# Performance work log

Hardware: AMD Instinct MI355X
Metric: run time of the kernel (lower is better)

## Reference

```python
import jax, jax.numpy as jnp
import numpy as np

NEG_SLOPE = 0.01  # torch F.leaky_relu default used in the DGL GAT-style layer


def grat_layer(h, src, dst, W, a, n_nodes):
    """One GRAT (GAT-style) layer.
    h: [N, d_in], src/dst: [E] int, W: [d_in, d_out], a: [2*d_out] (attn_fc weight
    on concat [z_src || z_dst]). Returns [N, d_out].
    """
    d_out = W.shape[1]
    z = h @ W                                   # [N, d_out]
    # attention logits per edge: a^T [z_src || z_dst]
    s_src = z @ a[:d_out]                       # [N]
    s_dst = z @ a[d_out:]                       # [N]
    e = jax.nn.leaky_relu(s_src[src] + s_dst[dst], NEG_SLOPE)  # [E]
    # numerically stable softmax over incoming edges of each dst node
    m = jax.ops.segment_max(e, dst, num_segments=n_nodes)      # [N]
    m = jnp.where(jnp.isfinite(m), m, 0.0)      # nodes with no in-edges
    w = jnp.exp(e - m[dst])                     # [E]
    denom = jax.ops.segment_sum(w, dst, num_segments=n_nodes)  # [N]
    alpha = w / jnp.maximum(denom, 1e-9)[dst]   # [E]
    # weighted scatter-aggregate of source features into dst
    out = jax.ops.segment_sum(alpha[:, None] * z[src], dst, num_segments=n_nodes)
    return out                                  # [N, d_out]


def setup_inputs() -> dict:
    key = jax.random.key(0)
    ks = jax.random.split(key, 10)
    N, E = 100000, 1600000
    IN, H1, H2, OUT = 128, 32, 32, 1
    feature = jax.random.normal(ks[0], (N, IN), dtype=jnp.float32)
    src = jax.random.randint(ks[1], (E,), 0, N, dtype=jnp.int32)
    dst = jax.random.randint(ks[2], (E,), 0, N, dtype=jnp.int32)
    s = 0.1
    W1 = jax.random.normal(ks[3], (IN, H1), dtype=jnp.float32) * s
    a1 = jax.random.normal(ks[4], (2 * H1,), dtype=jnp.float32) * s
    W2 = jax.random.normal(ks[5], (H1, H2), dtype=jnp.float32) * s
    a2 = jax.random.normal(ks[6], (2 * H2,), dtype=jnp.float32) * s
    W3 = jax.random.normal(ks[7], (H2, OUT), dtype=jnp.float32) * s
    a3 = jax.random.normal(ks[8], (2 * OUT,), dtype=jnp.float32) * s
    return {"feature": feature, "src": src, "dst": dst,
            "W1": W1, "a1": a1, "W2": W2, "a2": a2, "W3": W3, "a3": a3}


def reference(feature, src, dst, W1, a1, W2, a2, W3, a3):
    n = feature.shape[0]
    h = jax.nn.relu(grat_layer(feature, src, dst, W1, a1, n))
    h = jax.nn.relu(grat_layer(h, src, dst, W2, a2, n))
    h = grat_layer(h, src, dst, W3, a3, n)
    return jax.nn.sigmoid(h)                    # [N, 1]
```

## Files before the change

### kernel.cpp

```cpp
#include <hip/hip_runtime.h>
#include <hip/hip_bf16.h>
#include <cstdint>
#include <cstddef>

#define NEG_SLOPE 0.01f

static __device__ __forceinline__ unsigned short f2bf(float f) {
    __hip_bfloat16 b = __float2bfloat16(f);
    return *(unsigned short*)&b;
}
static __device__ __forceinline__ float bf2f(unsigned short u) {
    __hip_bfloat16 b = *(__hip_bfloat16*)&u;
    return __bfloat162float(b);
}


__global__ __launch_bounds__(128) void gemm1_kernel(
    const float* __restrict__ h, const float* __restrict__ W,
    const float* __restrict__ a, unsigned short* __restrict__ zb,
    float* __restrict__ s_src, float* __restrict__ s_dst, int N)
{
    __shared__ float Wl[128 * 32];
    int tid = threadIdx.x;
    int rowBase = blockIdx.x * 64;

    {
        const float4* W4 = (const float4*)W;
        float4* Wl4 = (float4*)Wl;
        for (int i = tid; i < 1024; i += 128) Wl4[i] = W4[i];
    }
    __syncthreads();

    int wv   = tid >> 6;
    int lane = tid & 63;
    int g    = lane >> 3;
    int l8   = lane & 7;
    int r0   = wv * 32 + g * 4;
    int col4 = l8 * 4;

    float acc[4][4];
#pragma unroll
    for (int i = 0; i < 4; i++)
#pragma unroll
        for (int c = 0; c < 4; c++) acc[i][c] = 0.f;

    const float4* h4  = (const float4*)h;
    const float4* Wl4 = (const float4*)Wl;

    size_t rowOff[4];
#pragma unroll
    for (int i = 0; i < 4; i++) {
        int r = rowBase + r0 + i;
        rowOff[i] = (size_t)((r < N) ? r : (N - 1)) * 32;
    }

#pragma unroll 2
    for (int kq = 0; kq < 32; kq++) {
        float4 w0 = Wl4[(kq * 4 + 0) * 8 + l8];
        float4 w1 = Wl4[(kq * 4 + 1) * 8 + l8];
        float4 w2 = Wl4[(kq * 4 + 2) * 8 + l8];
        float4 w3 = Wl4[(kq * 4 + 3) * 8 + l8];
#pragma unroll
        for (int i = 0; i < 4; i++) {
            float4 hv = h4[rowOff[i] + kq];
            acc[i][0] += hv.x * w0.x; acc[i][1] += hv.x * w0.y;
            acc[i][2] += hv.x * w0.z; acc[i][3] += hv.x * w0.w;
            acc[i][0] += hv.y * w1.x; acc[i][1] += hv.y * w1.y;
            acc[i][2] += hv.y * w1.z; acc[i][3] += hv.y * w1.w;
            acc[i][0] += hv.z * w2.x; acc[i][1] += hv.z * w2.y;
            acc[i][2] += hv.z * w2.z; acc[i][3] += hv.z * w2.w;
            acc[i][0] += hv.w * w3.x; acc[i][1] += hv.w * w3.y;
            acc[i][2] += hv.w * w3.z; acc[i][3] += hv.w * w3.w;
        }
    }

    float4 alo = ((const float4*)a)[l8];
    float4 ahi = ((const float4*)a)[8 + l8];
#pragma unroll
    for (int i = 0; i < 4; i++) {
        int row = rowBase + r0 + i;
        if (row < N) {
            ushort4 zv4 = make_ushort4(f2bf(acc[i][0]), f2bf(acc[i][1]),
                                       f2bf(acc[i][2]), f2bf(acc[i][3]));
            *(ushort4*)&zb[(size_t)row * 32 + col4] = zv4;
            float ps = acc[i][0] * alo.x + acc[i][1] * alo.y + acc[i][2] * alo.z + acc[i][3] * alo.w;
            float pd = acc[i][0] * ahi.x + acc[i][1] * ahi.y + acc[i][2] * ahi.z + acc[i][3] * ahi.w;
            ps += __shfl_xor(ps, 1, 64); ps += __shfl_xor(ps, 2, 64); ps += __shfl_xor(ps, 4, 64);
            pd += __shfl_xor(pd, 1, 64); pd += __shfl_xor(pd, 2, 64); pd += __shfl_xor(pd, 4, 64);
            if (l8 == 0) { s_src[row] = ps; s_dst[row] = pd; }
        }
    }
}

__global__ __launch_bounds__(128) void gemm2_kernel(
    const float* __restrict__ h, const float* __restrict__ W,
    const float* __restrict__ a, unsigned short* __restrict__ zb,
    float* __restrict__ s_src, float* __restrict__ s_dst, int N)
{
    __shared__ float Hl[64 * 44];
    __shared__ float Wl[32 * 32];
    int tid = threadIdx.x;
    int rowBase = blockIdx.x * 64;

    {
        const float4* W4 = (const float4*)W;
        float4* Wl4 = (float4*)Wl;
        for (int i = tid; i < 256; i += 128) Wl4[i] = W4[i];
    }
    {
        const float4* h4 = (const float4*)h;
        for (int i = tid; i < 64 * 8; i += 128) {
            int r = i >> 3, kq = i & 7;
            float4 v = (rowBase + r < N) ? h4[(size_t)(rowBase + r) * 8 + kq]
                                         : make_float4(0.f, 0.f, 0.f, 0.f);
            *(float4*)&Hl[r * 44 + kq * 4] = v;
        }
    }
    __syncthreads();

    int wv   = tid >> 6;
    int lane = tid & 63;
    int g    = lane >> 3;
    int l8   = lane & 7;
    int r0   = wv * 32 + g * 4;
    int col4 = l8 * 4;

    float acc[4][4];
#pragma unroll
    for (int i = 0; i < 4; i++)
#pragma unroll
        for (int c = 0; c < 4; c++) acc[i][c] = 0.f;

    const float4* H4  = (const float4*)Hl;
    const float4* Wl4 = (const float4*)Wl;

#pragma unroll
    for (int kq = 0; kq < 8; kq++) {
        float4 w0 = Wl4[(kq * 4 + 0) * 8 + l8];
        float4 w1 = Wl4[(kq * 4 + 1) * 8 + l8];
        float4 w2 = Wl4[(kq * 4 + 2) * 8 + l8];
        float4 w3 = Wl4[(kq * 4 + 3) * 8 + l8];
#pragma unroll
        for (int i = 0; i < 4; i++) {
            float4 hv = H4[(r0 + i) * 11 + kq];
            acc[i][0] += hv.x * w0.x; acc[i][1] += hv.x * w0.y;
            acc[i][2] += hv.x * w0.z; acc[i][3] += hv.x * w0.w;
            acc[i][0] += hv.y * w1.x; acc[i][1] += hv.y * w1.y;
            acc[i][2] += hv.y * w1.z; acc[i][3] += hv.y * w1.w;
            acc[i][0] += hv.z * w2.x; acc[i][1] += hv.z * w2.y;
            acc[i][2] += hv.z * w2.z; acc[i][3] += hv.z * w2.w;
            acc[i][0] += hv.w * w3.x; acc[i][1] += hv.w * w3.y;
            acc[i][2] += hv.w * w3.z; acc[i][3] += hv.w * w3.w;
        }
    }

    float4 alo = ((const float4*)a)[l8];
    float4 ahi = ((const float4*)a)[8 + l8];
#pragma unroll
    for (int i = 0; i < 4; i++) {
        int row = rowBase + r0 + i;
        if (row < N) {
            ushort4 zv4 = make_ushort4(f2bf(acc[i][0]), f2bf(acc[i][1]),
                                       f2bf(acc[i][2]), f2bf(acc[i][3]));
            *(ushort4*)&zb[(size_t)row * 32 + col4] = zv4;
            float ps = acc[i][0] * alo.x + acc[i][1] * alo.y + acc[i][2] * alo.z + acc[i][3] * alo.w;
            float pd = acc[i][0] * ahi.x + acc[i][1] * ahi.y + acc[i][2] * ahi.z + acc[i][3] * ahi.w;
            ps += __shfl_xor(ps, 1, 64); ps += __shfl_xor(ps, 2, 64); ps += __shfl_xor(ps, 4, 64);
            pd += __shfl_xor(pd, 1, 64); pd += __shfl_xor(pd, 2, 64); pd += __shfl_xor(pd, 4, 64);
            if (l8 == 0) { s_src[row] = ps; s_dst[row] = pd; }
        }
    }
}

__global__ __launch_bounds__(256) void gemm3_kernel(
    const float* __restrict__ h, const float* __restrict__ W,
    const float* __restrict__ a, float2* __restrict__ zs,
    float* __restrict__ s_dst, int N)
{
    int i = blockIdx.x * 256 + threadIdx.x;
    if (i >= N) return;
    const float4* hp = (const float4*)(h + (size_t)i * 32);
    const float4* wp = (const float4*)W;
    float acc = 0.f;
#pragma unroll
    for (int c = 0; c < 8; c++) {
        float4 v = hp[c];
        float4 w = wp[c];
        acc += v.x * w.x + v.y * w.y + v.z * w.z + v.w * w.w;
    }
    zs[i] = make_float2(acc, acc * a[0]);
    s_dst[i] = acc * a[1];
}


#define TILE_E 4096
#define NB_MAX 512

__global__ __launch_bounds__(256) void csr_hist_kernel(
    const int* __restrict__ dst, int* __restrict__ counts,
    int E, int TB, int NB)
{
    __shared__ int hist[NB_MAX];
    int tid = threadIdx.x;
    int t = blockIdx.x;
    for (int b = tid; b < NB; b += 256) hist[b] = 0;
    __syncthreads();
    int base = t * TILE_E;
    for (int i = tid; i < TILE_E; i += 256) {
        int k = base + i;
        if (k < E) atomicAdd(&hist[dst[k] >> 8], 1);
    }
    __syncthreads();
    for (int b = tid; b < NB; b += 256) counts[b * TB + t] = hist[b];
}

__global__ __launch_bounds__(256) void scan1_kernel(
    const int* __restrict__ vals, int* __restrict__ incl,
    int* __restrict__ blockSums, int M)
{
    __shared__ int tmp[256];
    int tid = threadIdx.x;
    int i = blockIdx.x * 256 + tid;
    int v = (i < M) ? vals[i] : 0;
    tmp[tid] = v;
    __syncthreads();
#pragma unroll
    for (int off = 1; off < 256; off <<= 1) {
        int t = (tid >= off) ? tmp[tid - off] : 0;
        __syncthreads();
        tmp[tid] += t;
        __syncthreads();
    }
    if (i < M) incl[i] = tmp[tid];
    if (tid == 255) blockSums[blockIdx.x] = tmp[255];
}

__global__ __launch_bounds__(1024) void scan2_kernel(int* __restrict__ blockSums, int nb)
{
    __shared__ int tmp[1024];
    int tid = threadIdx.x;
    int v = (tid < nb) ? blockSums[tid] : 0;
    tmp[tid] = v;
    __syncthreads();
#pragma unroll
    for (int off = 1; off < 1024; off <<= 1) {
        int t = (tid >= off) ? tmp[tid - off] : 0;
        __syncthreads();
        tmp[tid] += t;
        __syncthreads();
    }
    if (tid < nb) blockSums[tid] = tmp[tid] - v;
}

__global__ __launch_bounds__(256) void scan3_kernel(
    const int* __restrict__ vals, const int* __restrict__ blockSums,
    int* __restrict__ cscan, int M, int E)
{
    int i = blockIdx.x * 256 + threadIdx.x;
    if (i < M) {
        cscan[i] = cscan[i] - vals[i] + blockSums[i >> 8];
    }
    if (i == 0) cscan[M] = E;
}

__global__ __launch_bounds__(256) void csr_scatter_kernel(
    const int* __restrict__ src, const int* __restrict__ dst,
    const int* __restrict__ cscan, int* __restrict__ ebuf,
    int E, int TB, int NB)
{
    __shared__ int baseB[NB_MAX];
    __shared__ int cur[NB_MAX];
    int tid = threadIdx.x;
    int t = blockIdx.x;
    for (int b = tid; b < NB; b += 256) {
        baseB[b] = cscan[b * TB + t];
        cur[b] = 0;
    }
    __syncthreads();
    int base = t * TILE_E;
    for (int i = tid; i < TILE_E; i += 256) {
        int k = base + i;
        if (k < E) {
            int d = dst[k], s = src[k];
            int b = d >> 8;
            int r = atomicAdd(&cur[b], 1);
            ebuf[baseB[b] + r] = (s << 8) | (d & 255);
        }
    }
}

__global__ __launch_bounds__(256) void csr_bucket_kernel(
    const int* __restrict__ ebuf, const int* __restrict__ cscan,
    int* __restrict__ csr_src, int* __restrict__ offsets,
    int N, int E, int TB)
{
    __shared__ int eb[8192];
    __shared__ int hist[256];
    __shared__ int loff[256];
    __shared__ int tmp[256];
    int tid = threadIdx.x;
    int b = blockIdx.x;

    int beg = cscan[b * TB];
    int endv = cscan[(b + 1) * TB];
    int cnt = endv - beg;
    int first = b << 8;

    hist[tid] = 0;
    __syncthreads();

    bool inLds = (cnt <= 8192);
    for (int i = tid; i < cnt; i += 256) {
        int v = ebuf[beg + i];
        if (inLds) eb[i] = v;
        atomicAdd(&hist[v & 255], 1);
    }
    __syncthreads();

    int hv = hist[tid];
    tmp[tid] = hv;
    __syncthreads();
#pragma unroll
    for (int off = 1; off < 256; off <<= 1) {
        int t = (tid >= off) ? tmp[tid - off] : 0;
        __syncthreads();
        tmp[tid] += t;
        __syncthreads();
    }
    loff[tid] = tmp[tid] - hv;
    __syncthreads();

    if (first + tid < N) offsets[first + tid] = beg + loff[tid];
    if (b == 0 && tid == 0) offsets[N] = E;

    hist[tid] = 0;
    __syncthreads();

    for (int i = tid; i < cnt; i += 256) {
        int v = inLds ? eb[i] : ebuf[beg + i];
        int d8 = v & 255;
        int r = atomicAdd(&hist[d8], 1);
        csr_src[beg + loff[d8] + r] = v >> 8;
    }
}


__global__ __launch_bounds__(256) void agg32_fused_kernel(
    const int* __restrict__ offsets, const int* __restrict__ csr_src,
    const float* __restrict__ s_src, const float* __restrict__ s_dst,
    const unsigned short* __restrict__ zb, float* __restrict__ h, int N)
{
    __shared__ float2 wsbuf[8 * 128];
    int g    = threadIdx.x >> 5;
    int lane = threadIdx.x & 31;
    int node = blockIdx.x * 8 + g;
    if (node >= N) return;
    float2* ws = &wsbuf[g * 128];

    int beg = offsets[node], end = offsets[node + 1];
    int deg = end - beg;
    float sd = s_dst[node];
    float o = 0.f;
    float rden;

    if (deg <= 128) {
        int   sreg[4];
        float ev[4];
        int nIter = (deg + 31) >> 5;
        float m = -3.0e38f;
#pragma unroll 4
        for (int it = 0; it < nIter; ++it) {
            int p = beg + it * 32 + lane;
            float e = -3.0e38f;
            int s = 0;
            if (p < end) {
                s = csr_src[p];
                e = s_src[s] + sd;
                e = (e > 0.f) ? e : NEG_SLOPE * e;
            }
            sreg[it] = s;
            ev[it] = e;
            m = fmaxf(m, e);
        }
#pragma unroll
        for (int off = 16; off > 0; off >>= 1) m = fmaxf(m, __shfl_xor(m, off, 32));

        float l = 0.f;
#pragma unroll 4
        for (int it = 0; it < nIter; ++it) {
            int p = beg + it * 32 + lane;
            float w = (p < end) ? __expf(ev[it] - m) : 0.f;
            ws[it * 32 + lane] = make_float2(w, __int_as_float(sreg[it]));
            l += w;
        }
#pragma unroll
        for (int off = 16; off > 0; off >>= 1) l += __shfl_xor(l, off, 32);
        rden = 1.f / fmaxf(l, 1e-9f);

        int p = 0;
        for (; p + 4 <= deg; p += 4) {
            float2 a0 = ws[p],     a1 = ws[p + 1];
            float2 a2 = ws[p + 2], a3 = ws[p + 3];
            int s0 = __float_as_int(a0.y), s1 = __float_as_int(a1.y);
            int s2 = __float_as_int(a2.y), s3 = __float_as_int(a3.y);
            unsigned short u0 = zb[(size_t)s0 * 32 + lane];
            unsigned short u1 = zb[(size_t)s1 * 32 + lane];
            unsigned short u2 = zb[(size_t)s2 * 32 + lane];
            unsigned short u3 = zb[(size_t)s3 * 32 + lane];
            o += a0.x * bf2f(u0);
            o += a1.x * bf2f(u1);
            o += a2.x * bf2f(u2);
            o += a3.x * bf2f(u3);
        }
        for (; p < deg; ++p) {
            float2 aa = ws[p];
            o += aa.x * bf2f(zb[(size_t)__float_as_int(aa.y) * 32 + lane]);
        }
    } else {
        float m = -3.0e38f;
        for (int p = beg + lane; p < end; p += 32) {
            float e = s_src[csr_src[p]] + sd;
            e = (e > 0.f) ? e : NEG_SLOPE * e;
            m = fmaxf(m, e);
        }
#pragma unroll
        for (int off = 16; off > 0; off >>= 1) m = fmaxf(m, __shfl_xor(m, off, 32));
        float l = 0.f;
        for (int p = beg + lane; p < end; p += 32) {
            float e = s_src[csr_src[p]] + sd;
            e = (e > 0.f) ? e : NEG_SLOPE * e;
            l += __expf(e - m);
        }
#pragma unroll
        for (int off = 16; off > 0; off >>= 1) l += __shfl_xor(l, off, 32);
        rden = 1.f / fmaxf(l, 1e-9f);
        for (int p = beg; p < end; ++p) {
            int s = csr_src[p];
            float e = s_src[s] + sd;
            e = (e > 0.f) ? e : NEG_SLOPE * e;
            float w = __expf(e - m);
            o += w * bf2f(zb[(size_t)s * 32 + lane]);
        }
    }

    float v = o * rden;
    h[(size_t)node * 32 + lane] = (v > 0.f) ? v : 0.f;
}

__global__ __launch_bounds__(256) void agg1_fused_kernel(
    const int* __restrict__ offsets, const int* __restrict__ csr_src,
    const float2* __restrict__ zs, const float* __restrict__ s_dst,
    float* __restrict__ out, int N)
{
    int node = blockIdx.x * 8 + (threadIdx.x >> 5);
    int lane = threadIdx.x & 31;
    if (node >= N) return;

    int beg = offsets[node], end = offsets[node + 1];
    int deg = end - beg;
    float sd = s_dst[node];

    if (deg <= 128) {
        float ev[4], zv[4];
        int nIter = (deg + 31) >> 5;
        float m = -3.0e38f;
#pragma unroll 4
        for (int it = 0; it < nIter; ++it) {
            int p = beg + it * 32 + lane;
            float e = -3.0e38f, zz = 0.f;
            if (p < end) {
                float2 v2 = zs[csr_src[p]];
                zz = v2.x;
                e = v2.y + sd;
                e = (e > 0.f) ? e : NEG_SLOPE * e;
            }
            ev[it] = e; zv[it] = zz;
            m = fmaxf(m, e);
        }
#pragma unroll
        for (int off = 16; off > 0; off >>= 1) m = fmaxf(m, __shfl_xor(m, off, 32));
        float l = 0.f, o = 0.f;
#pragma unroll 4
        for (int it = 0; it < nIter; ++it) {
            int p = beg + it * 32 + lane;
            float w = (p < end) ? __expf(ev[it] - m) : 0.f;
            l += w;
            o += w * zv[it];
        }
#pragma unroll
        for (int off = 16; off > 0; off >>= 1) {
            l += __shfl_xor(l, off, 32);
            o += __shfl_xor(o, off, 32);
        }
        if (lane == 0) {
            float v = o / fmaxf(l, 1e-9f);
            out[node] = 1.f / (1.f + __expf(-v));
        }
    } else {
        float m = -3.0e38f;
        for (int p = beg + lane; p < end; p += 32) {
            float e = zs[csr_src[p]].y + sd;
            e = (e > 0.f) ? e : NEG_SLOPE * e;
            m = fmaxf(m, e);
        }
#pragma unroll
        for (int off = 16; off > 0; off >>= 1) m = fmaxf(m, __shfl_xor(m, off, 32));
        float l = 0.f, o = 0.f;
        for (int p = beg + lane; p < end; p += 32) {
            float2 v2 = zs[csr_src[p]];
            float e = v2.y + sd;
            e = (e > 0.f) ? e : NEG_SLOPE * e;
            float w = __expf(e - m);
            l += w; o += w * v2.x;
        }
#pragma unroll
        for (int off = 16; off > 0; off >>= 1) {
            l += __shfl_xor(l, off, 32);
            o += __shfl_xor(o, off, 32);
        }
        if (lane == 0) {
            float v = o / fmaxf(l, 1e-9f);
            out[node] = 1.f / (1.f + __expf(-v));
        }
    }
}


extern "C" void kernel_launch(void* const* d_in, const int* in_sizes, int n_in,
                              void* d_out, int out_size, void* d_ws, size_t ws_size,
                              hipStream_t stream)
{
    const float* feature = (const float*)d_in[0];
    const int*   src     = (const int*)d_in[1];
    const int*   dst     = (const int*)d_in[2];
    const float* W1      = (const float*)d_in[3];
    const float* a1      = (const float*)d_in[4];
    const float* W2      = (const float*)d_in[5];
    const float* a2      = (const float*)d_in[6];
    const float* W3      = (const float*)d_in[7];
    const float* a3      = (const float*)d_in[8];
    float* out = (float*)d_out;

    const int N = in_sizes[0] / 128;
    const int E = in_sizes[1];

    const int TB = (E + TILE_E - 1) / TILE_E;
    const int NB = (N + 255) >> 8;
    const int M  = NB * TB;

    char* p = (char*)d_ws;
    unsigned short* zb = (unsigned short*)p;  p += (size_t)N * 32 * sizeof(unsigned short);
    float* hbuf    = (float*)p;  p += (size_t)N * 32 * sizeof(float);
    float* zs32    = (float*)p;  p += (size_t)N * 2 * sizeof(float);
    float* s_src   = (float*)p;  p += (size_t)N * sizeof(float);
    float* s_dst   = (float*)p;  p += (size_t)N * sizeof(float);
    int*   offsets = (int*)p;    p += ((size_t)N + 1) * sizeof(int);
    int*   counts  = (int*)p;    p += ((size_t)M + 1) * sizeof(int);
    int*   cscan   = (int*)p;    p += ((size_t)M + 1) * sizeof(int);
    int*   blockSums = (int*)p;  p += 1024 * sizeof(int);
    int*   ebuf    = (int*)p;    p += (size_t)E * sizeof(int);
    int*   csr_src = (int*)p;    p += (size_t)E * sizeof(int);

    const int nodeBlocks8  = (N + 7) / 8;
    const int nodeBlocks   = (N + 255) / 256;
    const int gemmBlocks64 = (N + 63) / 64;
    const int scanBlocksM  = (M + 255) / 256;

    hipLaunchKernelGGL(csr_hist_kernel, dim3(TB), dim3(256), 0, stream,
                       dst, counts, E, TB, NB);
    hipLaunchKernelGGL(scan1_kernel, dim3(scanBlocksM), dim3(256), 0, stream,
                       counts, cscan, blockSums, M);
    hipLaunchKernelGGL(scan2_kernel, dim3(1), dim3(1024), 0, stream,
                       blockSums, scanBlocksM);
    hipLaunchKernelGGL(scan3_kernel, dim3(scanBlocksM), dim3(256), 0, stream,
                       counts, blockSums, cscan, M, E);
    hipLaunchKernelGGL(csr_scatter_kernel, dim3(TB), dim3(256), 0, stream,
                       src, dst, cscan, ebuf, E, TB, NB);
    hipLaunchKernelGGL(csr_bucket_kernel, dim3(NB), dim3(256), 0, stream,
                       ebuf, cscan, csr_src, offsets, N, E, TB);

    hipLaunchKernelGGL(gemm1_kernel, dim3(gemmBlocks64), dim3(128), 0, stream,
                       feature, W1, a1, zb, s_src, s_dst, N);
    hipLaunchKernelGGL(agg32_fused_kernel, dim3(nodeBlocks8), dim3(256), 0, stream,
                       offsets, csr_src, s_src, s_dst, zb, hbuf, N);

    hipLaunchKernelGGL(gemm2_kernel, dim3(gemmBlocks64), dim3(128), 0, stream,
                       hbuf, W2, a2, zb, s_src, s_dst, N);
    hipLaunchKernelGGL(agg32_fused_kernel, dim3(nodeBlocks8), dim3(256), 0, stream,
                       offsets, csr_src, s_src, s_dst, zb, hbuf, N);

    float2* zs = (float2*)zs32;
    hipLaunchKernelGGL(gemm3_kernel, dim3(nodeBlocks), dim3(256), 0, stream,
                       hbuf, W3, a3, zs, s_dst, N);
    hipLaunchKernelGGL(agg1_fused_kernel, dim3(nodeBlocks8), dim3(256), 0, stream,
                       offsets, csr_src, zs, s_dst, out, N);
}
```

Measured before the change: 276.8 us.

## Fuse next-layer GEMM and attention scores into aggregation kernel epilogues

The layer-2 and layer-3 GEMMs now run inside the layer-1 and layer-2 aggregation kernels. Each warp's aggregated, ReLU'd row is multiplied by W2 (staged in LDS) through lane shuffles, or reduced against W3. This removes two kernel launches and the write and re-read of the fp32 hidden buffer, using separate zb and score buffers per layer. The gather loop is also unrolled by 8 instead of 4, which adds register pressure and a block-wide LDS load of W2 plus a __syncthreads in the first aggregation kernel.

```diff
diff --git a/kernel.cpp b/kernel.cpp
--- a/kernel.cpp
+++ b/kernel.cpp
@@ -92,106 +92,6 @@
     }
 }
 
-__global__ __launch_bounds__(128) void gemm2_kernel(
-    const float* __restrict__ h, const float* __restrict__ W,
-    const float* __restrict__ a, unsigned short* __restrict__ zb,
-    float* __restrict__ s_src, float* __restrict__ s_dst, int N)
-{
-    __shared__ float Hl[64 * 44];
-    __shared__ float Wl[32 * 32];
-    int tid = threadIdx.x;
-    int rowBase = blockIdx.x * 64;
-
-    {
-        const float4* W4 = (const float4*)W;
-        float4* Wl4 = (float4*)Wl;
-        for (int i = tid; i < 256; i += 128) Wl4[i] = W4[i];
-    }
-    {
-        const float4* h4 = (const float4*)h;
-        for (int i = tid; i < 64 * 8; i += 128) {
-            int r = i >> 3, kq = i & 7;
-            float4 v = (rowBase + r < N) ? h4[(size_t)(rowBase + r) * 8 + kq]
-                                         : make_float4(0.f, 0.f, 0.f, 0.f);
-            *(float4*)&Hl[r * 44 + kq * 4] = v;
-        }
-    }
-    __syncthreads();
-
-    int wv   = tid >> 6;
-    int lane = tid & 63;
-    int g    = lane >> 3;
-    int l8   = lane & 7;
-    int r0   = wv * 32 + g * 4;
-    int col4 = l8 * 4;
-
-    float acc[4][4];
-#pragma unroll
-    for (int i = 0; i < 4; i++)
-#pragma unroll
-        for (int c = 0; c < 4; c++) acc[i][c] = 0.f;
-
-    const float4* H4  = (const float4*)Hl;
-    const float4* Wl4 = (const float4*)Wl;
-
-#pragma unroll
-    for (int kq = 0; kq < 8; kq++) {
-        float4 w0 = Wl4[(kq * 4 + 0) * 8 + l8];
-        float4 w1 = Wl4[(kq * 4 + 1) * 8 + l8];
-        float4 w2 = Wl4[(kq * 4 + 2) * 8 + l8];
-        float4 w3 = Wl4[(kq * 4 + 3) * 8 + l8];
-#pragma unroll
-        for (int i = 0; i < 4; i++) {
-            float4 hv = H4[(r0 + i) * 11 + kq];
-            acc[i][0] += hv.x * w0.x; acc[i][1] += hv.x * w0.y;
-            acc[i][2] += hv.x * w0.z; acc[i][3] += hv.x * w0.w;
-            acc[i][0] += hv.y * w1.x; acc[i][1] += hv.y * w1.y;
-            acc[i][2] += hv.y * w1.z; acc[i][3] += hv.y * w1.w;
-            acc[i][0] += hv.z * w2.x; acc[i][1] += hv.z * w2.y;
-            acc[i][2] += hv.z * w2.z; acc[i][3] += hv.z * w2.w;
-            acc[i][0] += hv.w * w3.x; acc[i][1] += hv.w * w3.y;
-            acc[i][2] += hv.w * w3.z; acc[i][3] += hv.w * w3.w;
-        }
-    }
-
-    float4 alo = ((const float4*)a)[l8];
-    float4 ahi = ((const float4*)a)[8 + l8];
-#pragma unroll
-    for (int i = 0; i < 4; i++) {
-        int row = rowBase + r0 + i;
-        if (row < N) {
-            ushort4 zv4 = make_ushort4(f2bf(acc[i][0]), f2bf(acc[i][1]),
-                                       f2bf(acc[i][2]), f2bf(acc[i][3]));
-            *(ushort4*)&zb[(size_t)row * 32 + col4] = zv4;
-            float ps = acc[i][0] * alo.x + acc[i][1] * alo.y + acc[i][2] * alo.z + acc[i][3] * alo.w;
-            float pd = acc[i][0] * ahi.x + acc[i][1] * ahi.y + acc[i][2] * ahi.z + acc[i][3] * ahi.w;
-            ps += __shfl_xor(ps, 1, 64); ps += __shfl_xor(ps, 2, 64); ps += __shfl_xor(ps, 4, 64);
-            pd += __shfl_xor(pd, 1, 64); pd += __shfl_xor(pd, 2, 64); pd += __shfl_xor(pd, 4, 64);
-            if (l8 == 0) { s_src[row] = ps; s_dst[row] = pd; }
-        }
-    }
-}
-
-__global__ __launch_bounds__(256) void gemm3_kernel(
-    const float* __restrict__ h, const float* __restrict__ W,
-    const float* __restrict__ a, float2* __restrict__ zs,
-    float* __restrict__ s_dst, int N)
-{
-    int i = blockIdx.x * 256 + threadIdx.x;
-    if (i >= N) return;
-    const float4* hp = (const float4*)(h + (size_t)i * 32);
-    const float4* wp = (const float4*)W;
-    float acc = 0.f;
-#pragma unroll
-    for (int c = 0; c < 8; c++) {
-        float4 v = hp[c];
-        float4 w = wp[c];
-        acc += v.x * w.x + v.y * w.y + v.z * w.z + v.w * w.w;
-    }
-    zs[i] = make_float2(acc, acc * a[0]);
-    s_dst[i] = acc * a[1];
-}
-
 
 #define TILE_E 4096
 #define NB_MAX 512
@@ -345,106 +245,161 @@
 }
 
 
-__global__ __launch_bounds__(256) void agg32_fused_kernel(
+#define AGG32_CORE(S_SRC, S_DST, ZB)                                          \
+    int beg = offsets[node], end = offsets[node + 1];                         \
+    int deg = end - beg;                                                      \
+    float sd = (S_DST)[node];                                                 \
+    float o = 0.f;                                                            \
+    float rden;                                                               \
+    if (deg <= 128) {                                                         \
+        int   sreg[4];                                                        \
+        float ev[4];                                                          \
+        int nIter = (deg + 31) >> 5;                                          \
+        float m = -3.0e38f;                                                   \
+        _Pragma("unroll 4")                                                   \
+        for (int it = 0; it < nIter; ++it) {                                  \
+            int p = beg + it * 32 + lane;                                     \
+            float e = -3.0e38f;                                               \
+            int s = 0;                                                        \
+            if (p < end) {                                                    \
+                s = csr_src[p];                                               \
+                e = (S_SRC)[s] + sd;                                          \
+                e = (e > 0.f) ? e : NEG_SLOPE * e;                            \
+            }                                                                 \
+            sreg[it] = s;                                                     \
+            ev[it] = e;                                                       \
+            m = fmaxf(m, e);                                                  \
+        }                                                                     \
+        _Pragma("unroll")                                                     \
+        for (int off = 16; off > 0; off >>= 1)                                \
+            m = fmaxf(m, __shfl_xor(m, off, 32));                             \
+        float l = 0.f;                                                        \
+        _Pragma("unroll 4")                                                   \
+        for (int it = 0; it < nIter; ++it) {                                  \
+            int p = beg + it * 32 + lane;                                     \
+            float w = (p < end) ? __expf(ev[it] - m) : 0.f;                   \
+            ws[it * 32 + lane] = make_float2(w, __int_as_float(sreg[it]));    \
+            l += w;                                                           \
+        }                                                                     \
+        _Pragma("unroll")                                                     \
+        for (int off = 16; off > 0; off >>= 1) l += __shfl_xor(l, off, 32);   \
+        rden = 1.f / fmaxf(l, 1e-9f);                                         \
+        int p = 0;                                                            \
+        for (; p + 8 <= deg; p += 8) {                                        \
+            float2 a0 = ws[p],     a1 = ws[p + 1];                            \
+            float2 a2 = ws[p + 2], a3 = ws[p + 3];                            \
+            float2 a4 = ws[p + 4], a5 = ws[p + 5];                            \
+            float2 a6 = ws[p + 6], a7 = ws[p + 7];                            \
+            unsigned short u0 = (ZB)[(size_t)__float_as_int(a0.y) * 32 + lane]; \
+            unsigned short u1 = (ZB)[(size_t)__float_as_int(a1.y) * 32 + lane]; \
+            unsigned short u2 = (ZB)[(size_t)__float_as_int(a2.y) * 32 + lane]; \
+            unsigned short u3 = (ZB)[(size_t)__float_as_int(a3.y) * 32 + lane]; \
+            unsigned short u4 = (ZB)[(size_t)__float_as_int(a4.y) * 32 + lane]; \
+            unsigned short u5 = (ZB)[(size_t)__float_as_int(a5.y) * 32 + lane]; \
+            unsigned short u6 = (ZB)[(size_t)__float_as_int(a6.y) * 32 + lane]; \
+            unsigned short u7 = (ZB)[(size_t)__float_as_int(a7.y) * 32 + lane]; \
+            o += a0.x * bf2f(u0); o += a1.x * bf2f(u1);                       \
+            o += a2.x * bf2f(u2); o += a3.x * bf2f(u3);                       \
+            o += a4.x * bf2f(u4); o += a5.x * bf2f(u5);                       \
+            o += a6.x * bf2f(u6); o += a7.x * bf2f(u7);                       \
+        }                                                                     \
+        for (; p < deg; ++p) {                                                \
+            float2 aa = ws[p];                                                \
+            o += aa.x * bf2f((ZB)[(size_t)__float_as_int(aa.y) * 32 + lane]); \
+        }                                                                     \
+    } else {                                                                  \
+        float m = -3.0e38f;                                                   \
+        for (int p = beg + lane; p < end; p += 32) {                          \
+            float e = (S_SRC)[csr_src[p]] + sd;                               \
+            e = (e > 0.f) ? e : NEG_SLOPE * e;                                \
+            m = fmaxf(m, e);                                                  \
+        }                                                                     \
+        _Pragma("unroll")                                                     \
+        for (int off = 16; off > 0; off >>= 1)                                \
+            m = fmaxf(m, __shfl_xor(m, off, 32));                             \
+        float l = 0.f;                                                        \
+        for (int p = beg + lane; p < end; p += 32) {                          \
+            float e = (S_SRC)[csr_src[p]] + sd;                               \
+            e = (e > 0.f) ? e : NEG_SLOPE * e;                                \
+            l += __expf(e - m);                                               \
+        }                                                                     \
+        _Pragma("unroll")                                                     \
+        for (int off = 16; off > 0; off >>= 1) l += __shfl_xor(l, off, 32);   \
+        rden = 1.f / fmaxf(l, 1e-9f);                                         \
+        for (int p = beg; p < end; ++p) {                                     \
+            int s = csr_src[p];                                               \
+            float e = (S_SRC)[s] + sd;                                        \
+            e = (e > 0.f) ? e : NEG_SLOPE * e;                                \
+            float w = __expf(e - m);                                          \
+            o += w * bf2f((ZB)[(size_t)s * 32 + lane]);                       \
+        }                                                                     \
+    }                                                                         \
+    float v = o * rden;                                                       \
+    v = (v > 0.f) ? v : 0.f;
+
+__global__ __launch_bounds__(256) void agg32_l1_kernel(
     const int* __restrict__ offsets, const int* __restrict__ csr_src,
-    const float* __restrict__ s_src, const float* __restrict__ s_dst,
-    const unsigned short* __restrict__ zb, float* __restrict__ h, int N)
-{
+    const float* __restrict__ s_src1, const float* __restrict__ s_dst1,
+    const unsigned short* __restrict__ zb1,
+    const float* __restrict__ W2, const float* __restrict__ a2,
+    unsigned short* __restrict__ zb2,
+    float* __restrict__ s_src2, float* __restrict__ s_dst2, int N)
+{
+    __shared__ float W2l[32 * 32];
     __shared__ float2 wsbuf[8 * 128];
-    int g    = threadIdx.x >> 5;
-    int lane = threadIdx.x & 31;
+    int tid = threadIdx.x;
+    for (int i = tid; i < 1024; i += 256) W2l[i] = W2[i];
+    __syncthreads();
+
+    int g    = tid >> 5;
+    int lane = tid & 31;
     int node = blockIdx.x * 8 + g;
     if (node >= N) return;
     float2* ws = &wsbuf[g * 128];
 
-    int beg = offsets[node], end = offsets[node + 1];
-    int deg = end - beg;
-    float sd = s_dst[node];
-    float o = 0.f;
-    float rden;
-
-    if (deg <= 128) {
-        int   sreg[4];
-        float ev[4];
-        int nIter = (deg + 31) >> 5;
-        float m = -3.0e38f;
-#pragma unroll 4
-        for (int it = 0; it < nIter; ++it) {
-            int p = beg + it * 32 + lane;
-            float e = -3.0e38f;
-            int s = 0;
-            if (p < end) {
-                s = csr_src[p];
-                e = s_src[s] + sd;
-                e = (e > 0.f) ? e : NEG_SLOPE * e;
-            }
-            sreg[it] = s;
-            ev[it] = e;
-            m = fmaxf(m, e);
-        }
-#pragma unroll
-        for (int off = 16; off > 0; off >>= 1) m = fmaxf(m, __shfl_xor(m, off, 32));
-
-        float l = 0.f;
-#pragma unroll 4
-        for (int it = 0; it < nIter; ++it) {
-            int p = beg + it * 32 + lane;
-            float w = (p < end) ? __expf(ev[it] - m) : 0.f;
-            ws[it * 32 + lane] = make_float2(w, __int_as_float(sreg[it]));
-            l += w;
-        }
-#pragma unroll
-        for (int off = 16; off > 0; off >>= 1) l += __shfl_xor(l, off, 32);
-        rden = 1.f / fmaxf(l, 1e-9f);
-
-        int p = 0;
-        for (; p + 4 <= deg; p += 4) {
-            float2 a0 = ws[p],     a1 = ws[p + 1];
-            float2 a2 = ws[p + 2], a3 = ws[p + 3];
-            int s0 = __float_as_int(a0.y), s1 = __float_as_int(a1.y);
-            int s2 = __float_as_int(a2.y), s3 = __float_as_int(a3.y);
-            unsigned short u0 = zb[(size_t)s0 * 32 + lane];
-            unsigned short u1 = zb[(size_t)s1 * 32 + lane];
-            unsigned short u2 = zb[(size_t)s2 * 32 + lane];
-            unsigned short u3 = zb[(size_t)s3 * 32 + lane];
-            o += a0.x * bf2f(u0);
-            o += a1.x * bf2f(u1);
-            o += a2.x * bf2f(u2);
-            o += a3.x * bf2f(u3);
-        }
-        for (; p < deg; ++p) {
-            float2 aa = ws[p];
-            o += aa.x * bf2f(zb[(size_t)__float_as_int(aa.y) * 32 + lane]);
-        }
-    } else {
-        float m = -3.0e38f;
-        for (int p = beg + lane; p < end; p += 32) {
-            float e = s_src[csr_src[p]] + sd;
-            e = (e > 0.f) ? e : NEG_SLOPE * e;
-            m = fmaxf(m, e);
-        }
-#pragma unroll
-        for (int off = 16; off > 0; off >>= 1) m = fmaxf(m, __shfl_xor(m, off, 32));
-        float l = 0.f;
-        for (int p = beg + lane; p < end; p += 32) {
-            float e = s_src[csr_src[p]] + sd;
-            e = (e > 0.f) ? e : NEG_SLOPE * e;
-            l += __expf(e - m);
-        }
-#pragma unroll
-        for (int off = 16; off > 0; off >>= 1) l += __shfl_xor(l, off, 32);
-        rden = 1.f / fmaxf(l, 1e-9f);
-        for (int p = beg; p < end; ++p) {
-            int s = csr_src[p];
-            float e = s_src[s] + sd;
-            e = (e > 0.f) ? e : NEG_SLOPE * e;
-            float w = __expf(e - m);
-            o += w * bf2f(zb[(size_t)s * 32 + lane]);
-        }
-    }
-
-    float v = o * rden;
-    h[(size_t)node * 32 + lane] = (v > 0.f) ? v : 0.f;
+    AGG32_CORE(s_src1, s_dst1, zb1)
+
+    float acc2 = 0.f;
+#pragma unroll
+    for (int k = 0; k < 32; ++k)
+        acc2 += __shfl(v, k, 32) * W2l[k * 32 + lane];
+
+    zb2[(size_t)node * 32 + lane] = f2bf(acc2);
+    float ps = acc2 * a2[lane];
+    float pd = acc2 * a2[32 + lane];
+#pragma unroll
+    for (int off = 16; off > 0; off >>= 1) {
+        ps += __shfl_xor(ps, off, 32);
+        pd += __shfl_xor(pd, off, 32);
+    }
+    if (lane == 0) { s_src2[node] = ps; s_dst2[node] = pd; }
+}
+
+__global__ __launch_bounds__(256) void agg32_l2_kernel(
+    const int* __restrict__ offsets, const int* __restrict__ csr_src,
+    const float* __restrict__ s_src2, const float* __restrict__ s_dst2,
+    const unsigned short* __restrict__ zb2,
+    const float* __restrict__ W3, const float* __restrict__ a3,
+    float2* __restrict__ zs, float* __restrict__ s_dst3, int N)
+{
+    __shared__ float2 wsbuf[8 * 128];
+    int tid  = threadIdx.x;
+    int g    = tid >> 5;
+    int lane = tid & 31;
+    int node = blockIdx.x * 8 + g;
+    if (node >= N) return;
+    float2* ws = &wsbuf[g * 128];
+    float w3 = W3[lane];
+
+    AGG32_CORE(s_src2, s_dst2, zb2)
+
+    float t = v * w3;
+#pragma unroll
+    for (int off = 16; off > 0; off >>= 1) t += __shfl_xor(t, off, 32);
+    if (lane == 0) {
+        zs[node] = make_float2(t, t * a3[0]);
+        s_dst3[node] = t * a3[1];
+    }
 }
 
 __global__ __launch_bounds__(256) void agg1_fused_kernel(
@@ -549,11 +504,14 @@
     const int M  = NB * TB;
 
     char* p = (char*)d_ws;
-    unsigned short* zb = (unsigned short*)p;  p += (size_t)N * 32 * sizeof(unsigned short);
-    float* hbuf    = (float*)p;  p += (size_t)N * 32 * sizeof(float);
+    unsigned short* zb1 = (unsigned short*)p;  p += (size_t)N * 32 * sizeof(unsigned short);
+    unsigned short* zb2 = (unsigned short*)p;  p += (size_t)N * 32 * sizeof(unsigned short);
     float* zs32    = (float*)p;  p += (size_t)N * 2 * sizeof(float);
-    float* s_src   = (float*)p;  p += (size_t)N * sizeof(float);
-    float* s_dst   = (float*)p;  p += (size_t)N * sizeof(float);
+    float* s_src1  = (float*)p;  p += (size_t)N * sizeof(float);
+    float* s_dst1  = (float*)p;  p += (size_t)N * sizeof(float);
+    float* s_src2  = (float*)p;  p += (size_t)N * sizeof(float);
+    float* s_dst2  = (float*)p;  p += (size_t)N * sizeof(float);
+    float* s_dst3  = (float*)p;  p += (size_t)N * sizeof(float);
     int*   offsets = (int*)p;    p += ((size_t)N + 1) * sizeof(int);
     int*   counts  = (int*)p;    p += ((size_t)M + 1) * sizeof(int);
     int*   cscan   = (int*)p;    p += ((size_t)M + 1) * sizeof(int);
@@ -562,7 +520,6 @@
     int*   csr_src = (int*)p;    p += (size_t)E * sizeof(int);
 
     const int nodeBlocks8  = (N + 7) / 8;
-    const int nodeBlocks   = (N + 255) / 256;
     const int gemmBlocks64 = (N + 63) / 64;
     const int scanBlocksM  = (M + 255) / 256;
 
@@ -580,18 +537,16 @@
                        ebuf, cscan, csr_src, offsets, N, E, TB);
 
     hipLaunchKernelGGL(gemm1_kernel, dim3(gemmBlocks64), dim3(128), 0, stream,
-                       feature, W1, a1, zb, s_src, s_dst, N);
-    hipLaunchKernelGGL(agg32_fused_kernel, dim3(nodeBlocks8), dim3(256), 0, stream,
-                       offsets, csr_src, s_src, s_dst, zb, hbuf, N);
-
-    hipLaunchKernelGGL(gemm2_kernel, dim3(gemmBlocks64), dim3(128), 0, stream,
-                       hbuf, W2, a2, zb, s_src, s_dst, N);
-    hipLaunchKernelGGL(agg32_fused_kernel, dim3(nodeBlocks8), dim3(256), 0, stream,
-                       offsets, csr_src, s_src, s_dst, zb, hbuf, N);
+                       feature, W1, a1, zb1, s_src1, s_dst1, N);
+    hipLaunchKernelGGL(agg32_l1_kernel, dim3(nodeBlocks8), dim3(256), 0, stream,
+                       offsets, csr_src, s_src1, s_dst1, zb1, W2, a2,
+                       zb2, s_src2, s_dst2, N);
 
     float2* zs = (float2*)zs32;
-    hipLaunchKernelGGL(gemm3_kernel, dim3(nodeBlocks), dim3(256), 0, stream,
-                       hbuf, W3, a3, zs, s_dst, N);
+    hipLaunchKernelGGL(agg32_l2_kernel, dim3(nodeBlocks8), dim3(256), 0, stream,
+                       offsets, csr_src, s_src2, s_dst2, zb2, W3, a3,
+                       zs, s_dst3, N);
+
     hipLaunchKernelGGL(agg1_fused_kernel, dim3(nodeBlocks8), dim3(256), 0, stream,
-                       offsets, csr_src, zs, s_dst, out, N);
-}
+                       offsets, csr_src, zs, s_dst3, out, N);
+}
```

Result: no change. 272.8 us (-1.5%).
